# Optimization experiments

Hardware: AMD Instinct MI355X
Metric: run time of the kernel (lower is better)

## Reference

```python
import jax, jax.numpy as jnp
import numpy as np

DIM = 128
HALF = DIM // 2
K = 8
B_TAIL = 1.0
MIN_W = 1e-3
MIN_H = 1e-3
MIN_D = 1e-3


def _fcnn(x, w1, b1, w2, b2, w3, b3):
    h = jax.nn.silu(x @ w1 + b1)
    h = jax.nn.silu(h @ w2 + b2)
    return h @ w3 + b3


def _rqs_forward(x, uw, uh, ud):
    # x: (B, D); uw/uh: (B, D, K); ud: (B, D, K-1)
    inside = (x >= -B_TAIL) & (x <= B_TAIL)
    const = np.log(np.exp(1.0 - MIN_D) - 1.0).astype(np.float32)
    ud = jnp.pad(ud, ((0, 0), (0, 0), (1, 1)), constant_values=const)

    widths = jax.nn.softmax(uw, axis=-1)
    widths = MIN_W + (1.0 - MIN_W * K) * widths
    cumw = jnp.pad(jnp.cumsum(widths, axis=-1), ((0, 0), (0, 0), (1, 0)))
    cumw = 2.0 * B_TAIL * cumw - B_TAIL
    cumw = cumw.at[..., 0].set(-B_TAIL).at[..., -1].set(B_TAIL)
    widths = cumw[..., 1:] - cumw[..., :-1]

    derivs = MIN_D + jax.nn.softplus(ud)

    heights = jax.nn.softmax(uh, axis=-1)
    heights = MIN_H + (1.0 - MIN_H * K) * heights
    cumh = jnp.pad(jnp.cumsum(heights, axis=-1), ((0, 0), (0, 0), (1, 0)))
    cumh = 2.0 * B_TAIL * cumh - B_TAIL
    cumh = cumh.at[..., 0].set(-B_TAIL).at[..., -1].set(B_TAIL)
    heights = cumh[..., 1:] - cumh[..., :-1]

    # searchsorted on cumwidths (forward direction)
    locs = cumw.at[..., -1].add(1e-6)
    idx = jnp.sum(x[..., None] >= locs, axis=-1) - 1
    idx = jnp.clip(idx, 0, K - 1)[..., None]  # (B, D, 1)

    g = lambda a: jnp.take_along_axis(a, idx, axis=-1)[..., 0]
    in_cumw = g(cumw)
    in_w = g(widths)
    in_cumh = g(cumh)
    in_h = g(heights)
    in_delta = g(heights / widths)
    d0 = g(derivs)
    d1 = g(derivs[..., 1:])

    theta = (x - in_cumw) / in_w
    t1mt = theta * (1.0 - theta)
    numer = in_h * (in_delta * theta * theta + d0 * t1mt)
    denom = in_delta + (d0 + d1 - 2.0 * in_delta) * t1mt
    out = in_cumh + numer / denom
    dnum = in_delta * in_delta * (d1 * theta * theta + 2.0 * in_delta * t1mt + d0 * (1.0 - theta) ** 2)
    lad = jnp.log(dnum) - 2.0 * jnp.log(denom)

    out = jnp.where(inside, out, x)
    lad = jnp.where(inside, lad, 0.0)
    return out, lad


def _forward(x, f1, f2):
    lower, upper = x[:, :HALF], x[:, HALF:]
    out = _fcnn(lower, *f1).reshape(-1, DIM - HALF, 3 * K - 1)
    W, H, D = out[..., :K], out[..., K:2 * K], out[..., 2 * K:]
    upper, ld1 = _rqs_forward(upper, W, H, D)
    out = _fcnn(upper, *f2).reshape(-1, HALF, 3 * K - 1)
    W, H, D = out[..., :K], out[..., K:2 * K], out[..., 2 * K:]
    lower, ld2 = _rqs_forward(lower, W, H, D)
    log_det = jnp.sum(ld1, axis=1) + jnp.sum(ld2, axis=1)
    return jnp.concatenate([lower, upper], axis=1), log_det


def setup_inputs() -> dict:
    key = jax.random.key(0)
    ks = jax.random.split(key, 13)
    batch = 32768
    x = jax.random.uniform(ks[0], (batch, DIM), jnp.float32, -1.2, 1.2)
    hd = 512
    out_dim = (3 * K - 1) * HALF  # 1472

    def lin(k, fan_in, fan_out):
        bound = 1.0 / np.sqrt(fan_in)
        kw, kb = jax.random.split(k)
        w = jax.random.uniform(kw, (fan_in, fan_out), jnp.float32, -bound, bound)
        b = jax.random.uniform(kb, (fan_out,), jnp.float32, -bound, bound)
        return w, b

    f1_w1, f1_b1 = lin(ks[1], HALF, hd)
    f1_w2, f1_b2 = lin(ks[2], hd, hd)
    f1_w3, f1_b3 = lin(ks[3], hd, out_dim)
    f2_w1, f2_b1 = lin(ks[4], HALF, hd)
    f2_w2, f2_b2 = lin(ks[5], hd, hd)
    f2_w3, f2_b3 = lin(ks[6], hd, out_dim)
    return dict(x=x,
                f1_w1=f1_w1, f1_b1=f1_b1, f1_w2=f1_w2, f1_b2=f1_b2, f1_w3=f1_w3, f1_b3=f1_b3,
                f2_w1=f2_w1, f2_b1=f2_b1, f2_w2=f2_w2, f2_b2=f2_b2, f2_w3=f2_w3, f2_b3=f2_b3)


def reference(x, f1_w1, f1_b1, f1_w2, f1_b2, f1_w3, f1_b3,
              f2_w1, f2_b1, f2_w2, f2_b2, f2_w3, f2_b3):
    f1 = (f1_w1, f1_b1, f1_w2, f1_b2, f1_w3, f1_b3)
    f2 = (f2_w1, f2_b1, f2_w2, f2_b2, f2_w3, f2_b3)
    return _forward(x, f1, f2)
```

## Files before the change

### kernel.cpp

```cpp
#include <hip/hip_runtime.h>

#define DIM 128
#define HALF 64

typedef __attribute__((ext_vector_type(8))) short bf16x8;
typedef __attribute__((ext_vector_type(4))) float f32x4;

static __device__ __forceinline__ float bf2f(unsigned int u16) {
    unsigned int v = u16 << 16;
    return __builtin_bit_cast(float, v);
}
static __device__ __forceinline__ unsigned short f2bf(float f) {
    unsigned int u = __builtin_bit_cast(unsigned int, f);
    unsigned int r = 0x7fffu + ((u >> 16) & 1u);
    u += r;
    return (unsigned short)(u >> 16);
}

static __device__ __forceinline__ void gload_lds16(const void* gptr, void* ldsptr) {
    __builtin_amdgcn_global_load_lds(
        (const __attribute__((address_space(1))) unsigned int*)(uintptr_t)gptr,
        (__attribute__((address_space(3))) unsigned int*)(unsigned int)(uintptr_t)ldsptr,
        16, 0, 0);
}


__global__ void conv_lower_kernel(const float* __restrict__ x,
                                  unsigned short* __restrict__ xl, int batch) {
    int i = blockIdx.x * 256 + threadIdx.x;
    if (i < batch * HALF) {
        int r = i >> 6, c = i & 63;
        xl[i] = f2bf(x[(size_t)r * DIM + c]);
    }
}

struct TransDesc {
    const float* src[6];
    unsigned short* dst[6];
};

__global__ void transpose_all_kernel(TransDesc d) {
    __shared__ float tile[32][33];
    int z = blockIdx.z;
    int K, BN, BK, Nin, pad24;
    switch (z) {
        case 0: case 3: K = 64;  BK = 2;  BN = 16; Nin = 512;  pad24 = 0; break;
        case 1: case 4: K = 512; BK = 16; BN = 16; Nin = 512;  pad24 = 0; break;
        default:        K = 512; BK = 16; BN = 48; Nin = 1472; pad24 = 1; break;
    }
    int bn = blockIdx.x, bk = blockIdx.y;
    if (bn >= BN || bk >= BK) return;
    const float* w = d.src[z];
    unsigned short* wt = d.dst[z];
    int tx = threadIdx.x, ty = threadIdx.y;
#pragma unroll
    for (int i = 0; i < 4; ++i) {
        int k = bk * 32 + ty + 8 * i;
        int n = bn * 32 + tx;
        float v = 0.f;
        if (pad24) {
            int g = n / 24, cc = n % 24;
            if (cc < 23) v = w[(size_t)k * Nin + (g * 23 + cc)];
        } else {
            v = w[(size_t)k * Nin + n];
        }
        tile[ty + 8 * i][tx] = v;
    }
    __syncthreads();
#pragma unroll
    for (int i = 0; i < 4; ++i) {
        int n = bn * 32 + ty + 8 * i;
        int k = bk * 32 + tx;
        wt[(size_t)n * K + k] = f2bf(tile[tx][ty + 8 * i]);
    }
}

template <bool SILU, bool PAD24, int NT>
__global__ __launch_bounds__(256, 4) void gemm_bf16_kernel(
    const unsigned short* __restrict__ A, const unsigned short* __restrict__ Bt,
    const float* __restrict__ bias, unsigned short* __restrict__ C,
    int M, int N, int K) {
    __shared__ __align__(16) unsigned char smem[34816];
    unsigned short* a_lds = (unsigned short*)smem;
    unsigned short* b_lds = (unsigned short*)(smem + 16384);
    unsigned short* cbuf = (unsigned short*)smem;

    const int t = threadIdx.x;
    const int lane = t & 63;
    const int wid = t >> 6;
    const int wr = wid >> 1, wc = wid & 1;

    const int nwg = gridDim.x;
    const int b = blockIdx.x;
    const int id = ((nwg & 7) == 0) ? ((b & 7) * (nwg >> 3) + (b >> 3)) : b;
    const int m0 = (id / NT) * 128;
    const int n0 = (id % NT) * 128;

    const int l15 = lane & 15;
    const int l4 = lane >> 4;
    const int srow = lane >> 3;
    const int sseg = lane & 7;
    const int sseg_swz = sseg ^ srow;
    const int rswz = (l15 & 7) * 8;

    f32x4 acc[4][4] = {};

    for (int kt = 0; kt < K; kt += 64) {
#pragma unroll
        for (int i = 0; i < 4; ++i) {
            int chunk = wid * 4 + i;
            int row = chunk * 8 + srow;
            const unsigned short* gA = A + (size_t)(m0 + row) * K + kt + sseg_swz * 8;
            const unsigned short* gB = Bt + (size_t)(n0 + row) * K + kt + sseg_swz * 8;
            gload_lds16(gA, &a_lds[chunk * 512]);
            gload_lds16(gB, &b_lds[chunk * 512]);
        }
        __syncthreads();
#pragma unroll
        for (int k0 = 0; k0 < 2; ++k0) {
            bf16x8 af[4], bfv[4];
#pragma unroll
            for (int f = 0; f < 4; ++f) {
                int col = (k0 * 32 + l4 * 8) ^ rswz;
                af[f] = *reinterpret_cast<const bf16x8*>(
                    &a_lds[(wr * 64 + f * 16 + l15) * 64 + col]);
                bfv[f] = *reinterpret_cast<const bf16x8*>(
                    &b_lds[(wc * 64 + f * 16 + l15) * 64 + col]);
            }
#pragma unroll
            for (int fm = 0; fm < 4; ++fm)
#pragma unroll
                for (int fn = 0; fn < 4; ++fn)
                    acc[fm][fn] = __builtin_amdgcn_mfma_f32_16x16x32_bf16(
                        af[fm], bfv[fn], acc[fm][fn], 0, 0, 0);
        }
        __syncthreads();
    }

    float bv[4];
#pragma unroll
    for (int fn = 0; fn < 4; ++fn) {
        int n = n0 + wc * 64 + fn * 16 + l15;
        if (PAD24) {
            int g = n / 24, cc = n % 24;
            bv[fn] = (cc < 23) ? bias[g * 23 + cc] : 0.f;
        } else {
            bv[fn] = bias[n];
        }
    }
#pragma unroll
    for (int fm = 0; fm < 4; ++fm) {
#pragma unroll
        for (int r = 0; r < 4; ++r) {
            int rl = wr * 64 + fm * 16 + l4 * 4 + r;
#pragma unroll
            for (int fn = 0; fn < 4; ++fn) {
                float v = acc[fm][fn][r] + bv[fn];
                if (SILU) v = v / (1.f + __expf(-v));
                cbuf[rl * 136 + wc * 64 + fn * 16 + l15] = f2bf(v);
            }
        }
    }
    __syncthreads();
#pragma unroll
    for (int p = 0; p < 8; ++p) {
        int unit = p * 256 + t;
        int row = unit >> 4, seg = unit & 15;
        uint4 v = *reinterpret_cast<const uint4*>(&cbuf[row * 136 + seg * 8]);
        *reinterpret_cast<uint4*>(&C[(size_t)(m0 + row) * N + n0 + seg * 8]) = v;
    }
}

__global__ __launch_bounds__(256, 1) void rqs_kernel(
        const float* __restrict__ x,
        const unsigned short* __restrict__ P,
        float* __restrict__ out, unsigned short* __restrict__ out_bf,
        float* __restrict__ ld_buf, float* __restrict__ logdet_out,
        int xoff, int pass, int batch) {
    const int wid = threadIdx.x >> 6;
    const int lane = threadIdx.x & 63;
    const int r = blockIdx.x * 4 + wid;
    if (r >= batch) return;

    const uint4* pv = reinterpret_cast<const uint4*>(P + (size_t)r * 1536 + lane * 24);
    uint4 q0 = pv[0], q1 = pv[1], q2 = pv[2];

    float W[8], H[8], Dv[7];
    {
        unsigned int a;
        a = q0.x; W[0] = bf2f(a & 0xffff); W[1] = bf2f(a >> 16);
        a = q0.y; W[2] = bf2f(a & 0xffff); W[3] = bf2f(a >> 16);
        a = q0.z; W[4] = bf2f(a & 0xffff); W[5] = bf2f(a >> 16);
        a = q0.w; W[6] = bf2f(a & 0xffff); W[7] = bf2f(a >> 16);
        a = q1.x; H[0] = bf2f(a & 0xffff); H[1] = bf2f(a >> 16);
        a = q1.y; H[2] = bf2f(a & 0xffff); H[3] = bf2f(a >> 16);
        a = q1.z; H[4] = bf2f(a & 0xffff); H[5] = bf2f(a >> 16);
        a = q1.w; H[6] = bf2f(a & 0xffff); H[7] = bf2f(a >> 16);
        a = q2.x; Dv[0] = bf2f(a & 0xffff); Dv[1] = bf2f(a >> 16);
        a = q2.y; Dv[2] = bf2f(a & 0xffff); Dv[3] = bf2f(a >> 16);
        a = q2.z; Dv[4] = bf2f(a & 0xffff); Dv[5] = bf2f(a >> 16);
        a = q2.w; Dv[6] = bf2f(a & 0xffff);
    }

    float cw[9], ch[9];
    {
        float m = W[0];
#pragma unroll
        for (int i = 1; i < 8; ++i) m = fmaxf(m, W[i]);
        float e[8], s = 0.f;
#pragma unroll
        for (int i = 0; i < 8; ++i) { e[i] = __expf(W[i] - m); s += e[i]; }
        float inv = __builtin_amdgcn_rcpf(s), cum = 0.f;
        cw[0] = -1.f;
#pragma unroll
        for (int i = 0; i < 8; ++i) {
            cum += 0.001f + 0.992f * e[i] * inv;
            cw[i + 1] = 2.f * cum - 1.f;
        }
        cw[8] = 1.f;
    }
    {
        float m = H[0];
#pragma unroll
        for (int i = 1; i < 8; ++i) m = fmaxf(m, H[i]);
        float e[8], s = 0.f;
#pragma unroll
        for (int i = 0; i < 8; ++i) { e[i] = __expf(H[i] - m); s += e[i]; }
        float inv = __builtin_amdgcn_rcpf(s), cum = 0.f;
        ch[0] = -1.f;
#pragma unroll
        for (int i = 0; i < 8; ++i) {
            cum += 0.001f + 0.992f * e[i] * inv;
            ch[i + 1] = 2.f * cum - 1.f;
        }
        ch[8] = 1.f;
    }
    float dv[9];
    dv[0] = 1.f; dv[8] = 1.f;
#pragma unroll
    for (int i = 0; i < 7; ++i) {
        float d = Dv[i];
        dv[i + 1] = 0.001f + fmaxf(d, 0.f) + __logf(1.f + __expf(-fabsf(d)));
    }

    const float xv = x[(size_t)r * DIM + xoff + lane];

    int cnt = (xv >= -1.f) ? 1 : 0;
#pragma unroll
    for (int i = 1; i < 8; ++i) cnt += (xv >= cw[i]) ? 1 : 0;
    cnt += (xv >= 1.000001f) ? 1 : 0;
    int idx = cnt - 1;
    idx = idx < 0 ? 0 : (idx > 7 ? 7 : idx);

    float in_cumw = -1.f, in_w = 1.f, in_cumh = -1.f, in_h = 1.f, d0 = 1.f, d1 = 1.f;
#pragma unroll
    for (int i = 0; i < 8; ++i) {
        bool s = (idx == i);
        float wi = cw[i + 1] - cw[i];
        float hi = ch[i + 1] - ch[i];
        in_cumw = s ? cw[i] : in_cumw;
        in_w = s ? wi : in_w;
        in_cumh = s ? ch[i] : in_cumh;
        in_h = s ? hi : in_h;
        d0 = s ? dv[i] : d0;
        d1 = s ? dv[i + 1] : d1;
    }

    float rw = __builtin_amdgcn_rcpf(in_w);
    float in_delta = in_h * rw;
    float theta = (xv - in_cumw) * rw;
    float omt = 1.f - theta;
    float t1mt = theta * omt;
    float numer = in_h * (in_delta * theta * theta + d0 * t1mt);
    float denom = in_delta + (d0 + d1 - 2.f * in_delta) * t1mt;
    float rd = __builtin_amdgcn_rcpf(denom);
    float outv = in_cumh + numer * rd;
    float dnum = in_delta * in_delta *
                 (d1 * theta * theta + 2.f * in_delta * t1mt + d0 * omt * omt);
    float lad = __logf(dnum * rd * rd);

    bool inside = (xv >= -1.f) && (xv <= 1.f);
    outv = inside ? outv : xv;
    lad = inside ? lad : 0.f;

    out[(size_t)r * DIM + xoff + lane] = outv;
    if (pass == 1) out_bf[(size_t)r * HALF + lane] = f2bf(outv);

#pragma unroll
    for (int off = 32; off > 0; off >>= 1) lad += __shfl_xor(lad, off);

    if (lane == 0) {
        if (pass == 1) ld_buf[r] = lad;
        else logdet_out[r] = lad + ld_buf[r];
    }
}


extern "C" void kernel_launch(void* const* d_in, const int* in_sizes, int n_in,
                              void* d_out, int out_size, void* d_ws, size_t ws_size,
                              hipStream_t stream) {
    const float* x = (const float*)d_in[0];
    const float* f1w1 = (const float*)d_in[1];
    const float* f1b1 = (const float*)d_in[2];
    const float* f1w2 = (const float*)d_in[3];
    const float* f1b2 = (const float*)d_in[4];
    const float* f1w3 = (const float*)d_in[5];
    const float* f1b3 = (const float*)d_in[6];
    const float* f2w1 = (const float*)d_in[7];
    const float* f2b1 = (const float*)d_in[8];
    const float* f2w2 = (const float*)d_in[9];
    const float* f2b2 = (const float*)d_in[10];
    const float* f2w3 = (const float*)d_in[11];
    const float* f2b3 = (const float*)d_in[12];
    const int batch = in_sizes[0] / DIM;
    float* out = (float*)d_out;

    char* ws = (char*)d_ws;
    size_t off = 0;
    auto alloc = [&](size_t bytes) -> void* {
        void* p = ws + off;
        off += (bytes + 255) & ~(size_t)255;
        return p;
    };
    unsigned short* xl = (unsigned short*)alloc((size_t)batch * 64 * 2);
    unsigned short* ub = (unsigned short*)alloc((size_t)batch * 64 * 2);
    unsigned short* w1t1 = (unsigned short*)alloc(512 * 64 * 2);
    unsigned short* w2t1 = (unsigned short*)alloc(512 * 512 * 2);
    unsigned short* w3t1 = (unsigned short*)alloc(1536 * 512 * 2);
    unsigned short* w1t2 = (unsigned short*)alloc(512 * 64 * 2);
    unsigned short* w2t2 = (unsigned short*)alloc(512 * 512 * 2);
    unsigned short* w3t2 = (unsigned short*)alloc(1536 * 512 * 2);
    unsigned short* h1 = (unsigned short*)alloc((size_t)batch * 512 * 2);
    unsigned short* h2 = (unsigned short*)alloc((size_t)batch * 512 * 2);
    unsigned short* par = (unsigned short*)alloc((size_t)batch * 1536 * 2);
    float* ld1 = (float*)alloc((size_t)batch * 4);
    (void)ws_size; (void)n_in; (void)out_size;

    conv_lower_kernel<<<(batch * 64 + 255) / 256, 256, 0, stream>>>(x, xl, batch);
    TransDesc td;
    td.src[0] = f1w1; td.dst[0] = w1t1;
    td.src[1] = f1w2; td.dst[1] = w2t1;
    td.src[2] = f1w3; td.dst[2] = w3t1;
    td.src[3] = f2w1; td.dst[3] = w1t2;
    td.src[4] = f2w2; td.dst[4] = w2t2;
    td.src[5] = f2w3; td.dst[5] = w3t2;
    transpose_all_kernel<<<dim3(48, 16, 6), dim3(32, 8), 0, stream>>>(td);

    dim3 blk(256);
    const int MB = batch / 128;
    gemm_bf16_kernel<true, false, 4><<<MB * 4, blk, 0, stream>>>(xl, w1t1, f1b1, h1, batch, 512, 64);
    gemm_bf16_kernel<true, false, 4><<<MB * 4, blk, 0, stream>>>(h1, w2t1, f1b2, h2, batch, 512, 512);
    gemm_bf16_kernel<false, true, 12><<<MB * 12, blk, 0, stream>>>(h2, w3t1, f1b3, par, batch, 1536, 512);
    rqs_kernel<<<batch / 4, 256, 0, stream>>>(x, par, out, ub, ld1, nullptr, HALF, 1, batch);
    gemm_bf16_kernel<true, false, 4><<<MB * 4, blk, 0, stream>>>(ub, w1t2, f2b1, h1, batch, 512, 64);
    gemm_bf16_kernel<true, false, 4><<<MB * 4, blk, 0, stream>>>(h1, w2t2, f2b2, h2, batch, 512, 512);
    gemm_bf16_kernel<false, true, 12><<<MB * 12, blk, 0, stream>>>(h2, w3t2, f2b3, par, batch, 1536, 512);
    rqs_kernel<<<batch / 4, 256, 0, stream>>>(x, par, out, nullptr, ld1, out + (size_t)batch * DIM, 0, 2, batch);
}
```

Before: 342.4 us.

## Add 256x128-tile GEMM with triple-buffered direct-to-LDS loads for K=512 layers

Adds a 512-thread GEMM kernel that computes 256x128 output tiles using a three-stage LDS ring filled by global_load_lds. Each K-step is split into two halves with interleaved prefetch, raw barriers, explicit waitcnts and raised priority around the MFMA blocks. The kernel is used for the hidden and output layers of both coupling MLPs, while the small K=64 first layer stays on the old kernel. The aim is to hide global-load latency and reuse A/B tiles more, at the cost of about 144KB of LDS per block, which limits occupancy, and more delicate hand-written synchronisation.

```diff
diff --git a/kernel.cpp b/kernel.cpp
--- a/kernel.cpp
+++ b/kernel.cpp
@@ -23,6 +23,11 @@
         (__attribute__((address_space(3))) unsigned int*)(unsigned int)(uintptr_t)ldsptr,
         16, 0, 0);
 }
+
+#define RAW_BARRIER()  __builtin_amdgcn_s_barrier()
+#define SCHED_FENCE()  __builtin_amdgcn_sched_barrier(0)
+#define WAIT_LGKM0()   asm volatile("s_waitcnt lgkmcnt(0)" ::: "memory")
+#define WAIT_VM(n)     asm volatile("s_waitcnt vmcnt(" #n ")" ::: "memory")
 
 
 __global__ void conv_lower_kernel(const float* __restrict__ x,
@@ -75,7 +80,7 @@
     }
 }
 
-template <bool SILU, bool PAD24, int NT>
+template <bool SILU, int NT>
 __global__ __launch_bounds__(256, 4) void gemm_bf16_kernel(
     const unsigned short* __restrict__ A, const unsigned short* __restrict__ Bt,
     const float* __restrict__ bias, unsigned short* __restrict__ C,
@@ -139,6 +144,136 @@
 
     float bv[4];
 #pragma unroll
+    for (int fn = 0; fn < 4; ++fn) bv[fn] = bias[n0 + wc * 64 + fn * 16 + l15];
+#pragma unroll
+    for (int fm = 0; fm < 4; ++fm) {
+#pragma unroll
+        for (int r = 0; r < 4; ++r) {
+            int rl = wr * 64 + fm * 16 + l4 * 4 + r;
+#pragma unroll
+            for (int fn = 0; fn < 4; ++fn) {
+                float v = acc[fm][fn][r] + bv[fn];
+                if (SILU) v = v / (1.f + __expf(-v));
+                cbuf[rl * 136 + wc * 64 + fn * 16 + l15] = f2bf(v);
+            }
+        }
+    }
+    __syncthreads();
+#pragma unroll
+    for (int p = 0; p < 8; ++p) {
+        int unit = p * 256 + t;
+        int row = unit >> 4, seg = unit & 15;
+        uint4 v = *reinterpret_cast<const uint4*>(&cbuf[row * 136 + seg * 8]);
+        *reinterpret_cast<uint4*>(&C[(size_t)(m0 + row) * N + n0 + seg * 8]) = v;
+    }
+}
+
+template <bool SILU, bool PAD24, int NT>
+__global__ __launch_bounds__(512, 2) void gemm256_kernel(
+    const unsigned short* __restrict__ A, const unsigned short* __restrict__ Bt,
+    const float* __restrict__ bias, unsigned short* __restrict__ C,
+    int M, int N, int K) {
+    __shared__ __align__(16) unsigned short lds[3 * 24576];
+
+    const int t = threadIdx.x;
+    const int lane = t & 63;
+    const int wid = t >> 6;
+    const int wr = wid >> 1;
+    const int wc = wid & 1;
+    const int l15 = lane & 15;
+    const int l4 = lane >> 4;
+    const int rswz = (l15 & 7) * 8;
+
+    const int nwg = gridDim.x;
+    const int b = blockIdx.x;
+    const int id = ((nwg & 7) == 0) ? ((b & 7) * (nwg >> 3) + (b >> 3)) : b;
+    const int m0 = (id / NT) * 256;
+    const int n0 = (id % NT) * 128;
+
+    const int rr = t >> 3;
+    const int seg8 = ((t & 7) ^ (rr & 7)) * 8;
+    const int nkt = K >> 6;
+
+    f32x4 acc[4][4] = {};
+
+    auto stageA = [&](int u, int j) {
+        unsigned short* dst = &lds[(u % 3) * 24576 + (j * 64 + wid * 8) * 64];
+        const unsigned short* src = A + (size_t)(m0 + j * 64 + rr) * K + u * 64 + seg8;
+        gload_lds16(src, dst);
+    };
+    auto stageB = [&](int u, int j) {
+        unsigned short* dst = &lds[(u % 3) * 24576 + 16384 + (j * 64 + wid * 8) * 64];
+        const unsigned short* src = Bt + (size_t)(n0 + j * 64 + rr) * K + u * 64 + seg8;
+        gload_lds16(src, dst);
+    };
+
+    stageA(0, 0); stageA(0, 1); stageA(0, 2); stageA(0, 3); stageB(0, 0); stageB(0, 1);
+    stageA(1, 0); stageA(1, 1); stageA(1, 2); stageA(1, 3); stageB(1, 0); stageB(1, 1);
+    WAIT_VM(6);
+    RAW_BARRIER();
+    SCHED_FENCE();
+
+    for (int kt = 0; kt < nkt; ++kt) {
+        const unsigned short* ab = &lds[(kt % 3) * 24576];
+        const unsigned short* bb = ab + 16384;
+        const bool st = (kt + 2 < nkt);
+
+        {
+            bf16x8 af[4], bfv[4];
+            const int col = (l4 * 8) ^ rswz;
+#pragma unroll
+            for (int f = 0; f < 4; ++f) {
+                af[f] = *reinterpret_cast<const bf16x8*>(
+                    &ab[(wr * 64 + f * 16 + l15) * 64 + col]);
+                bfv[f] = *reinterpret_cast<const bf16x8*>(
+                    &bb[(wc * 64 + f * 16 + l15) * 64 + col]);
+            }
+            if (st) { stageA(kt + 2, 0); stageA(kt + 2, 1); stageA(kt + 2, 2); }
+            RAW_BARRIER();
+            WAIT_LGKM0();
+            SCHED_FENCE();
+            __builtin_amdgcn_s_setprio(1);
+#pragma unroll
+            for (int fm = 0; fm < 4; ++fm)
+#pragma unroll
+                for (int fn = 0; fn < 4; ++fn)
+                    acc[fm][fn] = __builtin_amdgcn_mfma_f32_16x16x32_bf16(
+                        af[fm], bfv[fn], acc[fm][fn], 0, 0, 0);
+            __builtin_amdgcn_s_setprio(0);
+            RAW_BARRIER();
+            SCHED_FENCE();
+        }
+        {
+            bf16x8 af[4], bfv[4];
+            const int col = (32 + l4 * 8) ^ rswz;
+#pragma unroll
+            for (int f = 0; f < 4; ++f) {
+                af[f] = *reinterpret_cast<const bf16x8*>(
+                    &ab[(wr * 64 + f * 16 + l15) * 64 + col]);
+                bfv[f] = *reinterpret_cast<const bf16x8*>(
+                    &bb[(wc * 64 + f * 16 + l15) * 64 + col]);
+            }
+            if (st) { stageA(kt + 2, 3); stageB(kt + 2, 0); stageB(kt + 2, 1); }
+            RAW_BARRIER();
+            WAIT_LGKM0();
+            SCHED_FENCE();
+            __builtin_amdgcn_s_setprio(1);
+#pragma unroll
+            for (int fm = 0; fm < 4; ++fm)
+#pragma unroll
+                for (int fn = 0; fn < 4; ++fn)
+                    acc[fm][fn] = __builtin_amdgcn_mfma_f32_16x16x32_bf16(
+                        af[fm], bfv[fn], acc[fm][fn], 0, 0, 0);
+            __builtin_amdgcn_s_setprio(0);
+            if (st) { WAIT_VM(6); } else { WAIT_VM(0); }
+            RAW_BARRIER();
+            SCHED_FENCE();
+        }
+    }
+
+    unsigned short* cbuf = lds;
+    float bv[4];
+#pragma unroll
     for (int fn = 0; fn < 4; ++fn) {
         int n = n0 + wc * 64 + fn * 16 + l15;
         if (PAD24) {
@@ -164,7 +299,7 @@
     __syncthreads();
 #pragma unroll
     for (int p = 0; p < 8; ++p) {
-        int unit = p * 256 + t;
+        int unit = p * 512 + t;
         int row = unit >> 4, seg = unit & 15;
         uint4 v = *reinterpret_cast<const uint4*>(&cbuf[row * 136 + seg * 8]);
         *reinterpret_cast<uint4*>(&C[(size_t)(m0 + row) * N + n0 + seg * 8]) = v;
@@ -346,14 +481,14 @@
     td.src[5] = f2w3; td.dst[5] = w3t2;
     transpose_all_kernel<<<dim3(48, 16, 6), dim3(32, 8), 0, stream>>>(td);
 
-    dim3 blk(256);
-    const int MB = batch / 128;
-    gemm_bf16_kernel<true, false, 4><<<MB * 4, blk, 0, stream>>>(xl, w1t1, f1b1, h1, batch, 512, 64);
-    gemm_bf16_kernel<true, false, 4><<<MB * 4, blk, 0, stream>>>(h1, w2t1, f1b2, h2, batch, 512, 512);
-    gemm_bf16_kernel<false, true, 12><<<MB * 12, blk, 0, stream>>>(h2, w3t1, f1b3, par, batch, 1536, 512);
+    const int MB128 = batch / 128;
+    const int MB256 = batch / 256;
+    gemm_bf16_kernel<true, 4><<<MB128 * 4, 256, 0, stream>>>(xl, w1t1, f1b1, h1, batch, 512, 64);
+    gemm256_kernel<true, false, 4><<<MB256 * 4, 512, 0, stream>>>(h1, w2t1, f1b2, h2, batch, 512, 512);
+    gemm256_kernel<false, true, 12><<<MB256 * 12, 512, 0, stream>>>(h2, w3t1, f1b3, par, batch, 1536, 512);
     rqs_kernel<<<batch / 4, 256, 0, stream>>>(x, par, out, ub, ld1, nullptr, HALF, 1, batch);
-    gemm_bf16_kernel<true, false, 4><<<MB * 4, blk, 0, stream>>>(ub, w1t2, f2b1, h1, batch, 512, 64);
-    gemm_bf16_kernel<true, false, 4><<<MB * 4, blk, 0, stream>>>(h1, w2t2, f2b2, h2, batch, 512, 512);
-    gemm_bf16_kernel<false, true, 12><<<MB * 12, blk, 0, stream>>>(h2, w3t2, f2b3, par, batch, 1536, 512);
+    gemm_bf16_kernel<true, 4><<<MB128 * 4, 256, 0, stream>>>(ub, w1t2, f2b1, h1, batch, 512, 64);
+    gemm256_kernel<true, false, 4><<<MB256 * 4, 512, 0, stream>>>(h1, w2t2, f2b2, h2, batch, 512, 512);
+    gemm256_kernel<false, true, 12><<<MB256 * 12, 512, 0, stream>>>(h2, w3t2, f2b3, par, batch, 1536, 512);
     rqs_kernel<<<batch / 4, 256, 0, stream>>>(x, par, out, nullptr, ld1, out + (size_t)batch * DIM, 0, 2, batch);
 }
```

Result: slower. 399.9 us (+16.8%).

## Add 256x256-tile pipelined GEMM kernel for K=512 MLP layers

Applied to the files above, without the earlier changes.

Introduces a 512-thread GEMM kernel with 256x256 output tiles. It uses a four-stage asynchronous global-to-LDS load pipeline, explicit vmcnt waits with raw barriers, and raised wave priority during MFMA. The hidden and output layers of both coupling networks now use it, while the small K=64 first layer keeps the old kernel. The goal is more operand reuse per LDS byte and hiding load latency. In exchange, occupancy drops to one block per CU, and the grid for the hidden layer becomes small.

```diff
diff --git a/kernel.cpp b/kernel.cpp
--- a/kernel.cpp
+++ b/kernel.cpp
@@ -23,6 +23,10 @@
         (__attribute__((address_space(3))) unsigned int*)(unsigned int)(uintptr_t)ldsptr,
         16, 0, 0);
 }
+
+#define RAW_BARRIER()  __builtin_amdgcn_s_barrier()
+#define SCHED_FENCE()  __builtin_amdgcn_sched_barrier(0)
+#define WAIT_VM(n)     asm volatile("s_waitcnt vmcnt(" #n ")" ::: "memory")
 
 
 __global__ void conv_lower_kernel(const float* __restrict__ x,
@@ -75,7 +79,7 @@
     }
 }
 
-template <bool SILU, bool PAD24, int NT>
+template <bool SILU, int NT>
 __global__ __launch_bounds__(256, 4) void gemm_bf16_kernel(
     const unsigned short* __restrict__ A, const unsigned short* __restrict__ Bt,
     const float* __restrict__ bias, unsigned short* __restrict__ C,
@@ -139,6 +143,116 @@
 
     float bv[4];
 #pragma unroll
+    for (int fn = 0; fn < 4; ++fn) bv[fn] = bias[n0 + wc * 64 + fn * 16 + l15];
+#pragma unroll
+    for (int fm = 0; fm < 4; ++fm) {
+#pragma unroll
+        for (int r = 0; r < 4; ++r) {
+            int rl = wr * 64 + fm * 16 + l4 * 4 + r;
+#pragma unroll
+            for (int fn = 0; fn < 4; ++fn) {
+                float v = acc[fm][fn][r] + bv[fn];
+                if (SILU) v = v / (1.f + __expf(-v));
+                cbuf[rl * 136 + wc * 64 + fn * 16 + l15] = f2bf(v);
+            }
+        }
+    }
+    __syncthreads();
+#pragma unroll
+    for (int p = 0; p < 8; ++p) {
+        int unit = p * 256 + t;
+        int row = unit >> 4, seg = unit & 15;
+        uint4 v = *reinterpret_cast<const uint4*>(&cbuf[row * 136 + seg * 8]);
+        *reinterpret_cast<uint4*>(&C[(size_t)(m0 + row) * N + n0 + seg * 8]) = v;
+    }
+}
+
+template <bool SILU, bool PAD24, int NT>
+__global__ __launch_bounds__(512, 1) void gemm256_kernel(
+    const unsigned short* __restrict__ A, const unsigned short* __restrict__ Bt,
+    const float* __restrict__ bias, unsigned short* __restrict__ C,
+    int M, int N, int K) {
+    __shared__ __align__(16) unsigned short lds[256 * 264];
+
+    const int t = threadIdx.x;
+    const int lane = t & 63;
+    const int wid = t >> 6;
+    const int wr = wid >> 2;
+    const int wc = wid & 3;
+    const int l15 = lane & 15;
+    const int l4 = lane >> 4;
+
+    const int nwg = gridDim.x;
+    const int b = blockIdx.x;
+    const int id = ((nwg & 7) == 0) ? ((b & 7) * (nwg >> 3) + (b >> 3)) : b;
+    const int m0 = (id / NT) * 256;
+    const int n0 = (id % NT) * 256;
+
+    const int nkt = K >> 5;
+
+    int srow0 = t >> 2;
+    int srow1 = (512 + t) >> 2;
+    int sslot0 = (t & 3) ^ ((srow0 >> 1) & 3);
+    int sslot1 = (t & 3) ^ ((srow1 >> 1) & 3);
+    const int wbase0 = wid * 512;
+    const int wbase1 = 4096 + wid * 512;
+
+    f32x4 acc[8][4] = {};
+
+    auto stage = [&](int u) {
+        const int bi = (u & 3) * 16384;
+        const unsigned short* Au = A + (size_t)m0 * K + u * 32;
+        const unsigned short* Bu = Bt + (size_t)n0 * K + u * 32;
+        gload_lds16(Au + (size_t)srow0 * K + sslot0 * 8, &lds[bi + wbase0]);
+        gload_lds16(Au + (size_t)srow1 * K + sslot1 * 8, &lds[bi + wbase1]);
+        gload_lds16(Bu + (size_t)srow0 * K + sslot0 * 8, &lds[bi + 8192 + wbase0]);
+        gload_lds16(Bu + (size_t)srow1 * K + sslot1 * 8, &lds[bi + 8192 + wbase1]);
+    };
+
+    stage(0); stage(1); stage(2);
+    WAIT_VM(8);
+    RAW_BARRIER();
+    SCHED_FENCE();
+
+    for (int kt = 0; kt < nkt; ++kt) {
+        if (kt + 3 < nkt) stage(kt + 3);
+
+        const unsigned short* ab = &lds[(kt & 3) * 16384];
+        const unsigned short* bb = ab + 8192;
+
+        bf16x8 af[8], bfv[4];
+#pragma unroll
+        for (int f = 0; f < 8; ++f) {
+            int row = wr * 128 + f * 16 + l15;
+            int col = (l4 ^ ((row >> 1) & 3)) * 8;
+            af[f] = *reinterpret_cast<const bf16x8*>(&ab[row * 32 + col]);
+        }
+#pragma unroll
+        for (int f = 0; f < 4; ++f) {
+            int row = wc * 64 + f * 16 + l15;
+            int col = (l4 ^ ((row >> 1) & 3)) * 8;
+            bfv[f] = *reinterpret_cast<const bf16x8*>(&bb[row * 32 + col]);
+        }
+
+        __builtin_amdgcn_s_setprio(1);
+#pragma unroll
+        for (int fm = 0; fm < 8; ++fm)
+#pragma unroll
+            for (int fn = 0; fn < 4; ++fn)
+                acc[fm][fn] = __builtin_amdgcn_mfma_f32_16x16x32_bf16(
+                    af[fm], bfv[fn], acc[fm][fn], 0, 0, 0);
+        __builtin_amdgcn_s_setprio(0);
+
+        if (kt < nkt - 3) { WAIT_VM(8); }
+        else if (kt == nkt - 3) { WAIT_VM(4); }
+        else if (kt == nkt - 2) { WAIT_VM(0); }
+        RAW_BARRIER();
+        SCHED_FENCE();
+    }
+
+    unsigned short* cbuf = lds;
+    float bv[4];
+#pragma unroll
     for (int fn = 0; fn < 4; ++fn) {
         int n = n0 + wc * 64 + fn * 16 + l15;
         if (PAD24) {
@@ -149,24 +263,24 @@
         }
     }
 #pragma unroll
-    for (int fm = 0; fm < 4; ++fm) {
+    for (int fm = 0; fm < 8; ++fm) {
 #pragma unroll
         for (int r = 0; r < 4; ++r) {
-            int rl = wr * 64 + fm * 16 + l4 * 4 + r;
+            int rl = wr * 128 + fm * 16 + l4 * 4 + r;
 #pragma unroll
             for (int fn = 0; fn < 4; ++fn) {
                 float v = acc[fm][fn][r] + bv[fn];
                 if (SILU) v = v / (1.f + __expf(-v));
-                cbuf[rl * 136 + wc * 64 + fn * 16 + l15] = f2bf(v);
+                cbuf[rl * 264 + wc * 64 + fn * 16 + l15] = f2bf(v);
             }
         }
     }
     __syncthreads();
 #pragma unroll
-    for (int p = 0; p < 8; ++p) {
-        int unit = p * 256 + t;
-        int row = unit >> 4, seg = unit & 15;
-        uint4 v = *reinterpret_cast<const uint4*>(&cbuf[row * 136 + seg * 8]);
+    for (int p = 0; p < 16; ++p) {
+        int unit = p * 512 + t;
+        int row = unit >> 5, seg = unit & 31;
+        uint4 v = *reinterpret_cast<const uint4*>(&cbuf[row * 264 + seg * 8]);
         *reinterpret_cast<uint4*>(&C[(size_t)(m0 + row) * N + n0 + seg * 8]) = v;
     }
 }
@@ -346,14 +460,14 @@
     td.src[5] = f2w3; td.dst[5] = w3t2;
     transpose_all_kernel<<<dim3(48, 16, 6), dim3(32, 8), 0, stream>>>(td);
 
-    dim3 blk(256);
-    const int MB = batch / 128;
-    gemm_bf16_kernel<true, false, 4><<<MB * 4, blk, 0, stream>>>(xl, w1t1, f1b1, h1, batch, 512, 64);
-    gemm_bf16_kernel<true, false, 4><<<MB * 4, blk, 0, stream>>>(h1, w2t1, f1b2, h2, batch, 512, 512);
-    gemm_bf16_kernel<false, true, 12><<<MB * 12, blk, 0, stream>>>(h2, w3t1, f1b3, par, batch, 1536, 512);
+    const int MB128 = batch / 128;
+    const int MB256 = batch / 256;
+    gemm_bf16_kernel<true, 4><<<MB128 * 4, 256, 0, stream>>>(xl, w1t1, f1b1, h1, batch, 512, 64);
+    gemm256_kernel<true, false, 2><<<MB256 * 2, 512, 0, stream>>>(h1, w2t1, f1b2, h2, batch, 512, 512);
+    gemm256_kernel<false, true, 6><<<MB256 * 6, 512, 0, stream>>>(h2, w3t1, f1b3, par, batch, 1536, 512);
     rqs_kernel<<<batch / 4, 256, 0, stream>>>(x, par, out, ub, ld1, nullptr, HALF, 1, batch);
-    gemm_bf16_kernel<true, false, 4><<<MB * 4, blk, 0, stream>>>(ub, w1t2, f2b1, h1, batch, 512, 64);
-    gemm_bf16_kernel<true, false, 4><<<MB * 4, blk, 0, stream>>>(h1, w2t2, f2b2, h2, batch, 512, 512);
-    gemm_bf16_kernel<false, true, 12><<<MB * 12, blk, 0, stream>>>(h2, w3t2, f2b3, par, batch, 1536, 512);
+    gemm_bf16_kernel<true, 4><<<MB128 * 4, 256, 0, stream>>>(ub, w1t2, f2b1, h1, batch, 512, 64);
+    gemm256_kernel<true, false, 2><<<MB256 * 2, 512, 0, stream>>>(h1, w2t2, f2b2, h2, batch, 512, 512);
+    gemm256_kernel<false, true, 6><<<MB256 * 6, 512, 0, stream>>>(h2, w3t2, f2b3, par, batch, 1536, 512);
     rqs_kernel<<<batch / 4, 256, 0, stream>>>(x, par, out, nullptr, ld1, out + (size_t)batch * DIM, 0, 2, batch);
 }
```

After: 356.9 us. 1.04x slower.
